# Performance work log

Hardware: AMD Instinct MI355X
Metric: run time of the kernel (lower is better)

The kernel has to match this reference:

```python
import jax, jax.numpy as jnp
import numpy as np
import math

MAX_T = 1000

def _timestep_emb(t, emb_dim):
    half = emb_dim // 2
    freqs = jnp.exp(jnp.arange(half, dtype=jnp.float32) * -(math.log(MAX_T) / (half - 1)))
    e = t.astype(jnp.float32)[:, None] * freqs[None, :]
    return jnp.concatenate([jnp.sin(e), jnp.cos(e)], axis=1)  # [bs, emb_dim]


def setup_inputs() -> dict:
    key = jax.random.key(0)
    ks = jax.random.split(key, 12)
    BS, N, D, H = 16, 1024, 128, 8  # batch, nodes(=in_channels), out_dim(=d), heads
    w = lambda k, shape: jax.random.normal(k, shape, dtype=jnp.float32) * 0.05
    return {
        "A_t": jax.random.normal(ks[0], (BS, N, N), dtype=jnp.float32),
        "F_c": jax.random.normal(ks[1], (BS, N, D), dtype=jnp.float32),
        "t": jax.random.randint(ks[2], (BS,), 0, MAX_T),
        "Wq": w(ks[3], (D, D * H)), "bq": jnp.zeros((D * H,), jnp.float32),
        "Wk": w(ks[4], (D, D * H)), "bk": jnp.zeros((D * H,), jnp.float32),
        "Wv": w(ks[5], (D, D * H)), "bv": jnp.zeros((D * H,), jnp.float32),
        "Wo": w(ks[6], (D * H, D)), "bo": jnp.zeros((D,), jnp.float32),
        "Wg": jnp.eye(D, dtype=jnp.float32),  # GCN weight, eye init
    }


def reference(A_t, F_c, t, Wq, bq, Wk, bk, Wv, bv, Wo, bo, Wg):
    BS, N, D = F_c.shape
    H = Wq.shape[1] // D
    # timestep embedding, emb_dim = in_channels = N
    t_emb = _timestep_emb(t, N)                       # [bs, N]
    c = F_c + t_emb[:, :, None]                       # [bs, N, D]
    # naive multi-head self-attention with per-head dim = out_dim
    q = (c @ Wq + bq).reshape(BS, N, H, D).transpose(0, 2, 1, 3)
    k = (c @ Wk + bk).reshape(BS, N, H, D).transpose(0, 2, 1, 3)
    v = (c @ Wv + bv).reshape(BS, N, H, D).transpose(0, 2, 1, 3)
    scores = jnp.einsum('bhnd,bhmd->bhnm', q, k) / math.sqrt(D)
    a = jax.nn.softmax(scores, axis=-1)
    ctx = jnp.einsum('bhnm,bhmd->bhnd', a, v)
    ctx = ctx.transpose(0, 2, 1, 3).reshape(BS, N, H * D)
    h = ctx @ Wo + bo                                 # [bs, N, D]
    # GCN: relu(A @ (h @ W))
    feat = jax.nn.relu(A_t @ (h @ Wg))                # [bs, N, D]
    # Corr: row-normalize (unbiased std, matching torch.std) then bmm
    mu = feat.mean(axis=-1, keepdims=True)
    std = jnp.std(feat, axis=-1, ddof=1, keepdims=True)
    norm = (feat - mu) / (std + 1e-8)
    return jnp.einsum('bnd,bmd->bnm', norm, norm) / feat.shape[-1]
```

## Files before the change

kernel.cpp:

```cpp
#include <hip/hip_runtime.h>
#include <math.h>

#define NN 1024
#define DD 128
#define HH 8

typedef __attribute__((ext_vector_type(8))) short short8;
typedef __attribute__((ext_vector_type(4))) float f32x4;

__device__ inline unsigned short f2bf(float x) {
    union { float f; unsigned u; } v; v.f = x;
    return (unsigned short)((v.u + 0x7FFF + ((v.u >> 16) & 1)) >> 16);
}
__device__ inline unsigned pack2(float a, float b) {
    return (unsigned)f2bf(a) | ((unsigned)f2bf(b) << 16);
}

__global__ __launch_bounds__(256) void k_prep_w(
    const float* __restrict__ Wq, const float* __restrict__ Wk, const float* __restrict__ Wv,
    const float* __restrict__ Wo, const float* __restrict__ Wg,
    unsigned short* WqT, unsigned short* WkT, unsigned short* WvT,
    unsigned short* WoT, unsigned short* WgT) {
    int id = blockIdx.x;
    const float* src; unsigned short* dst; int R, C, ti;
    if (id < 128)      { src = Wq; dst = WqT; R = 128;  C = 1024; ti = id; }
    else if (id < 256) { src = Wk; dst = WkT; R = 128;  C = 1024; ti = id - 128; }
    else if (id < 384) { src = Wv; dst = WvT; R = 128;  C = 1024; ti = id - 256; }
    else if (id < 512) { src = Wo; dst = WoT; R = 1024; C = 128;  ti = id - 384; }
    else               { src = Wg; dst = WgT; R = 128;  C = 128;  ti = id - 512; }
    int tc = C >> 5;
    int r0 = (ti / tc) << 5, c0 = (ti % tc) << 5;
    __shared__ float T[32][33];
    int tid = threadIdx.x;
    int r = tid >> 3, c4 = (tid & 7) << 2;
    float4 v = *(const float4*)&src[(size_t)(r0 + r) * C + c0 + c4];
    T[r][c4] = v.x; T[r][c4 + 1] = v.y; T[r][c4 + 2] = v.z; T[r][c4 + 3] = v.w;
    __syncthreads();
    int c = tid >> 3, r4 = (tid & 7) << 2;
    uint2 o;
    o.x = pack2(T[r4][c], T[r4 + 1][c]);
    o.y = pack2(T[r4 + 2][c], T[r4 + 3][c]);
    *(uint2*)&dst[(size_t)(c0 + c) * R + r0 + r4] = o;
}

__global__ __launch_bounds__(256) void k_embed(const float* __restrict__ F_c,
                                               const int* __restrict__ t,
                                               unsigned short* __restrict__ cb) {
    int gi = blockIdx.x * 256 + threadIdx.x;
    int row = gi >> 4, ch = gi & 15;
    int b = row >> 10, n = row & 1023;
    float tv = (float)t[b];
    int j = n & 511;
    float e = tv * expf(-(float)j * 0.013518112092919054f);
    float emb = (n < 512) ? sinf(e) : cosf(e);
    const float* src = F_c + (size_t)row * 128 + ch * 8;
    float4 a = *(const float4*)src;
    float4 c4 = *(const float4*)(src + 4);
    uint4 o;
    o.x = pack2(a.x + emb, a.y + emb);  o.y = pack2(a.z + emb, a.w + emb);
    o.z = pack2(c4.x + emb, c4.y + emb); o.w = pack2(c4.z + emb, c4.w + emb);
    *(uint4*)&cb[(size_t)row * 128 + ch * 8] = o;
}

__device__ __forceinline__ void proj_body(const unsigned short* __restrict__ Ain,
                                          const unsigned short* __restrict__ WT,
                                          const float* __restrict__ bias,
                                          unsigned short* __restrict__ Out,
                                          float scale, int mode, int bh_mul,
                                          unsigned short* sm, int head, int m0) {
    unsigned short* CT  = sm;
    unsigned short* WTs = sm + 128 * 136;
    int tid = threadIdx.x;
    int w = tid >> 6, lane = tid & 63, n16 = lane & 15, quad = lane >> 4;
#pragma unroll
    for (int p = 0; p < 8; ++p) {
        int idx = tid + p * 256;
        int r = idx >> 4, ch = idx & 15;
        *(uint4*)&CT[r * 136 + ch * 8]  = *(const uint4*)&Ain[(size_t)(m0 + r) * 128 + ch * 8];
        *(uint4*)&WTs[r * 136 + ch * 8] = *(const uint4*)&WT[(size_t)(head * 128 + r) * 128 + ch * 8];
    }
    __syncthreads();
    int wr = (w >> 1) * 64, wc = (w & 1) * 64;
    f32x4 acc[4][4];
#pragma unroll
    for (int i = 0; i < 4; i++)
#pragma unroll
        for (int j = 0; j < 4; j++) acc[i][j] = (f32x4){0.f, 0.f, 0.f, 0.f};
#pragma unroll
    for (int kk = 0; kk < 4; ++kk) {
        short8 af[4], bf[4];
#pragma unroll
        for (int rb = 0; rb < 4; ++rb)
            af[rb] = *(const short8*)&CT[(wr + rb * 16 + n16) * 136 + kk * 32 + quad * 8];
#pragma unroll
        for (int cb = 0; cb < 4; ++cb)
            bf[cb] = *(const short8*)&WTs[(wc + cb * 16 + n16) * 136 + kk * 32 + quad * 8];
#pragma unroll
        for (int rb = 0; rb < 4; ++rb)
#pragma unroll
            for (int cb = 0; cb < 4; ++cb)
                acc[rb][cb] = __builtin_amdgcn_mfma_f32_16x16x32_bf16(af[rb], bf[cb], acc[rb][cb], 0, 0, 0);
    }
    __syncthreads();
#pragma unroll
    for (int rb = 0; rb < 4; ++rb)
#pragma unroll
        for (int cb = 0; cb < 4; ++cb) {
            int colb = wc + cb * 16 + n16;
            float bs = bias ? bias[head * 128 + colb] : 0.f;
#pragma unroll
            for (int reg = 0; reg < 4; ++reg) {
                int rowb = wr + rb * 16 + quad * 4 + reg;
                unsigned short val = f2bf((acc[rb][cb][reg] + bs) * scale);
                if (mode == 0) CT[rowb * 136 + colb] = val;
                else           CT[colb * 136 + rowb] = val;
            }
        }
    __syncthreads();
    int b = m0 >> 10, n0 = m0 & 1023;
    size_t base = (size_t)(b * bh_mul + head) * 131072;
    if (mode == 0) {
#pragma unroll
        for (int p = 0; p < 8; ++p) {
            int idx = tid + p * 256;
            int r = idx >> 4, ch = idx & 15;
            *(uint4*)&Out[base + (size_t)(n0 + r) * 128 + ch * 8] = *(const uint4*)&CT[r * 136 + ch * 8];
        }
    } else {
#pragma unroll
        for (int p = 0; p < 8; ++p) {
            int idx = tid + p * 256;
            int r = idx >> 4, ch = idx & 15;
            *(uint4*)&Out[base + (size_t)r * 1024 + n0 + ch * 8] = *(const uint4*)&CT[r * 136 + ch * 8];
        }
    }
}

__global__ __launch_bounds__(256) void k_proj_qkv(const unsigned short* __restrict__ Ain,
                                                  const unsigned short* __restrict__ W0,
                                                  const unsigned short* __restrict__ W1,
                                                  const unsigned short* __restrict__ W2,
                                                  const float* __restrict__ b0,
                                                  const float* __restrict__ b1,
                                                  const float* __restrict__ b2,
                                                  unsigned short* __restrict__ O0,
                                                  unsigned short* __restrict__ O1,
                                                  unsigned short* __restrict__ O2,
                                                  float qscale) {
    __shared__ __align__(16) unsigned short sm[2 * 128 * 136];
    int z = blockIdx.z;
    const unsigned short* WT = (z == 0) ? W0 : (z == 1) ? W1 : W2;
    const float* bias = (z == 0) ? b0 : (z == 1) ? b1 : b2;
    unsigned short* Out = (z == 0) ? O0 : (z == 1) ? O1 : O2;
    float scale = (z == 0) ? qscale : 1.f;
    int mode = (z == 2) ? 1 : 0;
    proj_body(Ain, WT, bias, Out, scale, mode, 8, sm, blockIdx.y, blockIdx.x * 128);
}

__global__ __launch_bounds__(256) void k_proj(const unsigned short* __restrict__ Ain,
                                              const unsigned short* __restrict__ WT,
                                              const float* __restrict__ bias,
                                              unsigned short* __restrict__ Out,
                                              float scale, int mode, int bh_mul) {
    __shared__ __align__(16) unsigned short sm[2 * 128 * 136];
    proj_body(Ain, WT, bias, Out, scale, mode, bh_mul, sm, blockIdx.y, blockIdx.x * 128);
}

__device__ __forceinline__ void attn_compute(const unsigned short* __restrict__ Ksc,
                                             const unsigned short* __restrict__ Vtc,
                                             const short8 (&qf)[2][4],
                                             float (&mrun)[2], float (&lrun)[2],
                                             f32x4 (&O)[2][8], int n16, int quad) {
    f32x4 S[2][4];
#pragma unroll
    for (int qb2 = 0; qb2 < 2; ++qb2)
#pragma unroll
        for (int kb = 0; kb < 4; ++kb) S[qb2][kb] = (f32x4){0.f, 0.f, 0.f, 0.f};
    __builtin_amdgcn_s_setprio(1);
#pragma unroll
    for (int kb = 0; kb < 4; ++kb)
#pragma unroll
        for (int dc = 0; dc < 4; ++dc) {
            short8 kf = *(const short8*)&Ksc[(kb * 16 + n16) * 136 + dc * 32 + quad * 8];
            S[0][kb] = __builtin_amdgcn_mfma_f32_16x16x32_bf16(kf, qf[0][dc], S[0][kb], 0, 0, 0);
            S[1][kb] = __builtin_amdgcn_mfma_f32_16x16x32_bf16(kf, qf[1][dc], S[1][kb], 0, 0, 0);
        }
    __builtin_amdgcn_s_setprio(0);

    float mx[2];
#pragma unroll
    for (int qb2 = 0; qb2 < 2; ++qb2) {
        float m = S[qb2][0][0];
#pragma unroll
        for (int kb = 0; kb < 4; ++kb)
#pragma unroll
            for (int reg = 0; reg < 4; ++reg) m = fmaxf(m, S[qb2][kb][reg]);
        m = fmaxf(m, __shfl_xor(m, 16));
        m = fmaxf(m, __shfl_xor(m, 32));
        mx[qb2] = m;
    }
    int keep = (mx[0] - mrun[0] <= 1.f) && (mx[1] - mrun[1] <= 1.f);
    if (!__all(keep)) {
        float mn0 = fmaxf(mrun[0], mx[0]);
        float mn1 = fmaxf(mrun[1], mx[1]);
        float a0 = __expf(mrun[0] - mn0);
        float a1 = __expf(mrun[1] - mn1);
        mrun[0] = mn0; mrun[1] = mn1;
        lrun[0] *= a0; lrun[1] *= a1;
        float av0[4], av1[4];
#pragma unroll
        for (int reg = 0; reg < 4; ++reg) {
            av0[reg] = __shfl(a0, quad * 4 + reg);
            av1[reg] = __shfl(a1, quad * 4 + reg);
        }
#pragma unroll
        for (int dc = 0; dc < 8; ++dc)
#pragma unroll
            for (int reg = 0; reg < 4; ++reg) {
                O[0][dc][reg] *= av0[reg];
                O[1][dc][reg] *= av1[reg];
            }
    }
#pragma unroll
    for (int qb2 = 0; qb2 < 2; ++qb2) {
        float ps = 0.f;
#pragma unroll
        for (int kb = 0; kb < 4; ++kb)
#pragma unroll
            for (int reg = 0; reg < 4; ++reg) {
                float p = __expf(S[qb2][kb][reg] - mrun[qb2]);
                S[qb2][kb][reg] = p;
                ps += p;
            }
        ps += __shfl_xor(ps, 16);
        ps += __shfl_xor(ps, 32);
        lrun[qb2] += ps;
    }
    unsigned pk01[2][4], pk23[2][4];
#pragma unroll
    for (int qb2 = 0; qb2 < 2; ++qb2)
#pragma unroll
        for (int kb = 0; kb < 4; ++kb) {
            asm("v_cvt_pk_bf16_f32 %0, %1, %2"
                : "=v"(pk01[qb2][kb]) : "v"(S[qb2][kb][0]), "v"(S[qb2][kb][1]));
            asm("v_cvt_pk_bf16_f32 %0, %1, %2"
                : "=v"(pk23[qb2][kb]) : "v"(S[qb2][kb][2]), "v"(S[qb2][kb][3]));
        }
    __builtin_amdgcn_s_setprio(1);
#pragma unroll
    for (int c = 0; c < 2; ++c) {
        union { uint4 u; short8 s; } pa0, pa1;
        pa0.u = make_uint4(pk01[0][2 * c], pk23[0][2 * c], pk01[0][2 * c + 1], pk23[0][2 * c + 1]);
        pa1.u = make_uint4(pk01[1][2 * c], pk23[1][2 * c], pk01[1][2 * c + 1], pk23[1][2 * c + 1]);
#pragma unroll
        for (int dc = 0; dc < 8; ++dc) {
            short8 vf = *(const short8*)&Vtc[(dc * 16 + n16) * 72 + c * 32 + quad * 8];
            O[0][dc] = __builtin_amdgcn_mfma_f32_16x16x32_bf16(pa0.s, vf, O[0][dc], 0, 0, 0);
            O[1][dc] = __builtin_amdgcn_mfma_f32_16x16x32_bf16(pa1.s, vf, O[1][dc], 0, 0, 0);
        }
    }
    __builtin_amdgcn_s_setprio(0);
}

__global__ __launch_bounds__(256, 2) void k_attn2(const unsigned short* __restrict__ qbuf,
                                                  const unsigned short* __restrict__ kbuf,
                                                  const unsigned short* __restrict__ vtb,
                                                  unsigned short* __restrict__ ctxb) {
    __shared__ __align__(16) unsigned short sm[35840];
    const int tid = threadIdx.x;
    const int w = tid >> 6, lane = tid & 63;
    const int n16 = lane & 15, quad = lane >> 4;
    const int g = blockIdx.x;
    const int bh = g & 127, tileq = g >> 7;

    const unsigned short* Qp = qbuf + (size_t)bh * 131072 + (size_t)tileq * 16384;
    const unsigned short* Kp = kbuf + (size_t)bh * 131072;
    const unsigned short* Vp = vtb + (size_t)bh * 131072;

    short8 qf[2][4];
#pragma unroll
    for (int qb2 = 0; qb2 < 2; ++qb2)
#pragma unroll
        for (int dc = 0; dc < 4; ++dc)
            qf[qb2][dc] = *(const short8*)&Qp[(size_t)(w * 32 + qb2 * 16 + n16) * 128 + dc * 32 + quad * 8];

    float mrun[2] = {-1e30f, -1e30f};
    float lrun[2] = {0.f, 0.f};
    f32x4 O[2][8];
#pragma unroll
    for (int qb2 = 0; qb2 < 2; ++qb2)
#pragma unroll
        for (int dc = 0; dc < 8; ++dc) O[qb2][dc] = (f32x4){0.f, 0.f, 0.f, 0.f};

    const int vr0 = tid >> 3;
    const int k0 = (tid & 7) * 8;
    const int slotA = ((k0 >> 5) << 5) | (((k0 >> 2) & 3) << 3) | (((k0 >> 4) & 1) << 2);

    uint4 ka[4], va[4];
#pragma unroll
    for (int p = 0; p < 4; ++p) {
        int idx = tid + p * 256;
        int r = idx >> 4, ch = idx & 15;
        ka[p] = *(const uint4*)&Kp[(size_t)r * 128 + ch * 8];
        va[p] = *(const uint4*)&Vp[(size_t)(vr0 + p * 32) * 1024 + k0];
    }
    {
        unsigned short* Kw = sm;
        unsigned short* Vw = sm + 8704;
#pragma unroll
        for (int p = 0; p < 4; ++p) {
            int idx = tid + p * 256;
            int r = idx >> 4, ch = idx & 15;
            *(uint4*)&Kw[r * 136 + ch * 8] = ka[p];
        }
#pragma unroll
        for (int p = 0; p < 4; ++p) {
            int r = vr0 + p * 32;
            *(uint2*)&Vw[r * 72 + slotA]     = make_uint2(va[p].x, va[p].y);
            *(uint2*)&Vw[r * 72 + slotA + 8] = make_uint2(va[p].z, va[p].w);
        }
    }
    __syncthreads();

    for (int kt = 0; kt < 16; ++kt) {
        if (kt < 15) {
#pragma unroll
            for (int p = 0; p < 4; ++p) {
                int idx = tid + p * 256;
                int r = idx >> 4, ch = idx & 15;
                ka[p] = *(const uint4*)&Kp[(size_t)((kt + 1) * 64 + r) * 128 + ch * 8];
                va[p] = *(const uint4*)&Vp[(size_t)(vr0 + p * 32) * 1024 + (kt + 1) * 64 + k0];
            }
        }
        {
            const unsigned short* Ksc = sm + (kt & 1) * 17920;
            const unsigned short* Vtc = Ksc + 8704;
            attn_compute(Ksc, Vtc, qf, mrun, lrun, O, n16, quad);
        }
        if (kt < 15) {
            unsigned short* Kw = sm + ((kt + 1) & 1) * 17920;
            unsigned short* Vw = Kw + 8704;
#pragma unroll
            for (int p = 0; p < 4; ++p) {
                int idx = tid + p * 256;
                int r = idx >> 4, ch = idx & 15;
                *(uint4*)&Kw[r * 136 + ch * 8] = ka[p];
            }
#pragma unroll
            for (int p = 0; p < 4; ++p) {
                int r = vr0 + p * 32;
                *(uint2*)&Vw[r * 72 + slotA]     = make_uint2(va[p].x, va[p].y);
                *(uint2*)&Vw[r * 72 + slotA + 8] = make_uint2(va[p].z, va[p].w);
            }
        }
        __syncthreads();
    }

    float lv[2][4];
#pragma unroll
    for (int qb2 = 0; qb2 < 2; ++qb2)
#pragma unroll
        for (int reg = 0; reg < 4; ++reg)
            lv[qb2][reg] = 1.f / __shfl(lrun[qb2], quad * 4 + reg);
    unsigned short* Ct = sm;
#pragma unroll
    for (int qb2 = 0; qb2 < 2; ++qb2)
#pragma unroll
        for (int reg = 0; reg < 4; ++reg) {
            int row = w * 32 + qb2 * 16 + quad * 4 + reg;
#pragma unroll
            for (int dc = 0; dc < 8; ++dc)
                Ct[row * 136 + dc * 16 + n16] = f2bf(O[qb2][dc][reg] * lv[qb2][reg]);
        }
    __syncthreads();
    unsigned short* Outp = ctxb + (size_t)bh * 131072 + (size_t)tileq * 16384;
#pragma unroll
    for (int p = 0; p < 8; ++p) {
        int idx = tid + p * 256;
        int r = idx >> 4, ch = idx & 15;
        *(uint4*)&Outp[(size_t)r * 128 + ch * 8] = *(const uint4*)&Ct[r * 136 + ch * 8];
    }
}

__global__ __launch_bounds__(256) void k_proj_o(const unsigned short* __restrict__ Ctxb,
                                                const unsigned short* __restrict__ WoT,
                                                const float* __restrict__ bo,
                                                unsigned short* __restrict__ Hb) {
    __shared__ __align__(16) unsigned short sm[2 * 13824];
    int tid = threadIdx.x;
    int m0 = blockIdx.x * 64;
    int b = m0 >> 10, n0 = m0 & 1023;
    int w = tid >> 6, lane = tid & 63, n16 = lane & 15, quad = lane >> 4;
    int wr = (w & 1) * 32, wc = (w >> 1) * 64;
    int r8 = tid >> 3, ch8 = tid & 7;
    f32x4 acc[2][4];
#pragma unroll
    for (int i = 0; i < 2; i++)
#pragma unroll
        for (int j = 0; j < 4; j++) acc[i][j] = (f32x4){0.f, 0.f, 0.f, 0.f};
    uint4 aR[2], bR[4];
#pragma unroll
    for (int p = 0; p < 2; ++p)
        aR[p] = *(const uint4*)&Ctxb[((size_t)(b * 8) * 1024 + n0 + r8 + p * 32) * 128 + ch8 * 8];
#pragma unroll
    for (int p = 0; p < 4; ++p)
        bR[p] = *(const uint4*)&WoT[(size_t)(r8 + p * 32) * 1024 + ch8 * 8];
    {
        unsigned short* As = sm;
        unsigned short* Bs = sm + 64 * 72;
#pragma unroll
        for (int p = 0; p < 2; ++p) *(uint4*)&As[(r8 + p * 32) * 72 + ch8 * 8] = aR[p];
#pragma unroll
        for (int p = 0; p < 4; ++p) *(uint4*)&Bs[(r8 + p * 32) * 72 + ch8 * 8] = bR[p];
    }
    __syncthreads();
    for (int kt = 0; kt < 16; ++kt) {
        if (kt < 15) {
            int kn = kt + 1, hh = kn >> 1, d0 = (kn & 1) * 64;
#pragma unroll
            for (int p = 0; p < 2; ++p)
                aR[p] = *(const uint4*)&Ctxb[((size_t)(b * 8 + hh) * 1024 + n0 + r8 + p * 32) * 128 + d0 + ch8 * 8];
#pragma unroll
            for (int p = 0; p < 4; ++p)
                bR[p] = *(const uint4*)&WoT[(size_t)(r8 + p * 32) * 1024 + kn * 64 + ch8 * 8];
        }
        const unsigned short* As = sm + (kt & 1) * 13824;
        const unsigned short* Bs = As + 64 * 72;
#pragma unroll
        for (int kk = 0; kk < 2; ++kk) {
            short8 af0 = *(const short8*)&As[(wr + n16) * 72 + kk * 32 + quad * 8];
            short8 af1 = *(const short8*)&As[(wr + 16 + n16) * 72 + kk * 32 + quad * 8];
#pragma unroll
            for (int cb = 0; cb < 4; ++cb) {
                short8 bf = *(const short8*)&Bs[(wc + cb * 16 + n16) * 72 + kk * 32 + quad * 8];
                acc[0][cb] = __builtin_amdgcn_mfma_f32_16x16x32_bf16(af0, bf, acc[0][cb], 0, 0, 0);
                acc[1][cb] = __builtin_amdgcn_mfma_f32_16x16x32_bf16(af1, bf, acc[1][cb], 0, 0, 0);
            }
        }
        if (kt < 15) {
            unsigned short* Aw = sm + ((kt + 1) & 1) * 13824;
            unsigned short* Bw = Aw + 64 * 72;
#pragma unroll
            for (int p = 0; p < 2; ++p) *(uint4*)&Aw[(r8 + p * 32) * 72 + ch8 * 8] = aR[p];
#pragma unroll
            for (int p = 0; p < 4; ++p) *(uint4*)&Bw[(r8 + p * 32) * 72 + ch8 * 8] = bR[p];
        }
        __syncthreads();
    }
    unsigned short* Ct = sm;
#pragma unroll
    for (int rb = 0; rb < 2; ++rb)
#pragma unroll
        for (int cb = 0; cb < 4; ++cb) {
            int col = wc + cb * 16 + n16;
            float bs = bo[col];
#pragma unroll
            for (int reg = 0; reg < 4; ++reg)
                Ct[(wr + rb * 16 + quad * 4 + reg) * 136 + col] = f2bf(acc[rb][cb][reg] + bs);
        }
    __syncthreads();
#pragma unroll
    for (int p = 0; p < 4; ++p) {
        int idx = tid + p * 256;
        int r = idx >> 4, ch = idx & 15;
        *(uint4*)&Hb[(size_t)(m0 + r) * 128 + ch * 8] = *(const uint4*)&Ct[r * 136 + ch * 8];
    }
}

__global__ __launch_bounds__(256) void k_at_gemm(const float* __restrict__ At,
                                                 const unsigned short* __restrict__ HgT,
                                                 float* __restrict__ Feat) {
    __shared__ __align__(16) unsigned short sm[2 * 13824];
    int tid = threadIdx.x;
    int bz = blockIdx.z;
    int m0 = blockIdx.x * 64;
    int w = tid >> 6, lane = tid & 63, n16 = lane & 15, quad = lane >> 4;
    int wr = (w & 1) * 32, wc = (w >> 1) * 64;
    int r8 = tid >> 3, ch8 = tid & 7;
    f32x4 acc[2][4];
#pragma unroll
    for (int i = 0; i < 2; i++)
#pragma unroll
        for (int j = 0; j < 4; j++) acc[i][j] = (f32x4){0.f, 0.f, 0.f, 0.f};
    float4 axR[2], ayR[2]; uint4 bR[4];
#pragma unroll
    for (int p = 0; p < 2; ++p) {
        const float* s = At + (size_t)bz * 1048576 + (size_t)(m0 + r8 + p * 32) * 1024 + ch8 * 8;
        axR[p] = *(const float4*)s;
        ayR[p] = *(const float4*)(s + 4);
    }
#pragma unroll
    for (int p = 0; p < 4; ++p)
        bR[p] = *(const uint4*)&HgT[(size_t)bz * 131072 + (size_t)(r8 + p * 32) * 1024 + ch8 * 8];
    {
        unsigned short* As = sm;
        unsigned short* Bs = sm + 64 * 72;
#pragma unroll
        for (int p = 0; p < 2; ++p) {
            uint4 o;
            o.x = pack2(axR[p].x, axR[p].y); o.y = pack2(axR[p].z, axR[p].w);
            o.z = pack2(ayR[p].x, ayR[p].y); o.w = pack2(ayR[p].z, ayR[p].w);
            *(uint4*)&As[(r8 + p * 32) * 72 + ch8 * 8] = o;
        }
#pragma unroll
        for (int p = 0; p < 4; ++p) *(uint4*)&Bs[(r8 + p * 32) * 72 + ch8 * 8] = bR[p];
    }
    __syncthreads();
    for (int kt = 0; kt < 16; ++kt) {
        if (kt < 15) {
            int kn = kt + 1;
#pragma unroll
            for (int p = 0; p < 2; ++p) {
                const float* s = At + (size_t)bz * 1048576 + (size_t)(m0 + r8 + p * 32) * 1024 + kn * 64 + ch8 * 8;
                axR[p] = *(const float4*)s;
                ayR[p] = *(const float4*)(s + 4);
            }
#pragma unroll
            for (int p = 0; p < 4; ++p)
                bR[p] = *(const uint4*)&HgT[(size_t)bz * 131072 + (size_t)(r8 + p * 32) * 1024 + kn * 64 + ch8 * 8];
        }
        const unsigned short* As = sm + (kt & 1) * 13824;
        const unsigned short* Bs = As + 64 * 72;
#pragma unroll
        for (int kk = 0; kk < 2; ++kk) {
            short8 af0 = *(const short8*)&As[(wr + n16) * 72 + kk * 32 + quad * 8];
            short8 af1 = *(const short8*)&As[(wr + 16 + n16) * 72 + kk * 32 + quad * 8];
#pragma unroll
            for (int cb = 0; cb < 4; ++cb) {
                short8 bf = *(const short8*)&Bs[(wc + cb * 16 + n16) * 72 + kk * 32 + quad * 8];
                acc[0][cb] = __builtin_amdgcn_mfma_f32_16x16x32_bf16(af0, bf, acc[0][cb], 0, 0, 0);
                acc[1][cb] = __builtin_amdgcn_mfma_f32_16x16x32_bf16(af1, bf, acc[1][cb], 0, 0, 0);
            }
        }
        if (kt < 15) {
            unsigned short* Aw = sm + ((kt + 1) & 1) * 13824;
            unsigned short* Bw = Aw + 64 * 72;
#pragma unroll
            for (int p = 0; p < 2; ++p) {
                uint4 o;
                o.x = pack2(axR[p].x, axR[p].y); o.y = pack2(axR[p].z, axR[p].w);
                o.z = pack2(ayR[p].x, ayR[p].y); o.w = pack2(ayR[p].z, ayR[p].w);
                *(uint4*)&Aw[(r8 + p * 32) * 72 + ch8 * 8] = o;
            }
#pragma unroll
            for (int p = 0; p < 4; ++p) *(uint4*)&Bw[(r8 + p * 32) * 72 + ch8 * 8] = bR[p];
        }
        __syncthreads();
    }
#pragma unroll
    for (int rb = 0; rb < 2; ++rb)
#pragma unroll
        for (int cb = 0; cb < 4; ++cb) {
            int col = wc + cb * 16 + n16;
#pragma unroll
            for (int reg = 0; reg < 4; ++reg) {
                int row = m0 + wr + rb * 16 + quad * 4 + reg;
                Feat[(size_t)bz * 131072 + (size_t)row * 128 + col] = fmaxf(acc[rb][cb][reg], 0.f);
            }
        }
}

__global__ __launch_bounds__(64) void k_norm(const float* __restrict__ F,
                                             unsigned short* __restrict__ Nb) {
    int row = blockIdx.x, tdx = threadIdx.x;
    const float* p = F + (size_t)row * 128;
    float2 xy = *(const float2*)&p[tdx * 2];
    float sum = xy.x + xy.y;
#pragma unroll
    for (int off = 32; off; off >>= 1) sum += __shfl_xor(sum, off);
    float mu = sum * (1.f / 128.f);
    float d0 = xy.x - mu, d1 = xy.y - mu;
    float sq = d0 * d0 + d1 * d1;
#pragma unroll
    for (int off = 32; off; off >>= 1) sq += __shfl_xor(sq, off);
    float sd = sqrtf(sq * (1.f / 127.f));
    float inv = 1.f / (sd + 1e-8f);
    ((unsigned*)Nb)[(size_t)row * 64 + tdx] = pack2(d0 * inv, d1 * inv);
}

__global__ __launch_bounds__(256) void k_corr(const unsigned short* __restrict__ Nb,
                                              float* __restrict__ Out) {
    __shared__ __align__(16) unsigned short sm[2 * 128 * 136];
    unsigned short* Ar = sm;
    unsigned short* Br = sm + 128 * 136;
    int tid = threadIdx.x;
    int bz = blockIdx.z;
    int n0 = blockIdx.x * 128, m0 = blockIdx.y * 128;
    const unsigned short* base = Nb + (size_t)bz * 131072;
    int w = tid >> 6, lane = tid & 63, n16 = lane & 15, quad = lane >> 4;
#pragma unroll
    for (int p = 0; p < 8; ++p) {
        int idx = tid + p * 256;
        int r = idx >> 4, ch = idx & 15;
        *(uint4*)&Ar[r * 136 + ch * 8] = *(const uint4*)&base[(size_t)(n0 + r) * 128 + ch * 8];
        *(uint4*)&Br[r * 136 + ch * 8] = *(const uint4*)&base[(size_t)(m0 + r) * 128 + ch * 8];
    }
    __syncthreads();
    int wr = (w >> 1) * 64, wc = (w & 1) * 64;
    f32x4 acc[4][4];
#pragma unroll
    for (int i = 0; i < 4; i++)
#pragma unroll
        for (int j = 0; j < 4; j++) acc[i][j] = (f32x4){0.f, 0.f, 0.f, 0.f};
#pragma unroll
    for (int kk = 0; kk < 4; ++kk) {
        short8 af[4], bf[4];
#pragma unroll
        for (int rb = 0; rb < 4; ++rb)
            af[rb] = *(const short8*)&Ar[(wr + rb * 16 + n16) * 136 + kk * 32 + quad * 8];
#pragma unroll
        for (int cb = 0; cb < 4; ++cb)
            bf[cb] = *(const short8*)&Br[(wc + cb * 16 + n16) * 136 + kk * 32 + quad * 8];
#pragma unroll
        for (int rb = 0; rb < 4; ++rb)
#pragma unroll
            for (int cb = 0; cb < 4; ++cb)
                acc[rb][cb] = __builtin_amdgcn_mfma_f32_16x16x32_bf16(af[rb], bf[cb], acc[rb][cb], 0, 0, 0);
    }
#pragma unroll
    for (int rb = 0; rb < 4; ++rb)
#pragma unroll
        for (int cb = 0; cb < 4; ++cb)
#pragma unroll
            for (int reg = 0; reg < 4; ++reg) {
                int row = n0 + wr + rb * 16 + quad * 4 + reg;
                int col = m0 + wc + cb * 16 + n16;
                Out[(size_t)bz * 1048576 + (size_t)row * 1024 + col] = acc[rb][cb][reg] * 0.0078125f;
            }
}

extern "C" void kernel_launch(void* const* d_in, const int* in_sizes, int n_in,
                              void* d_out, int out_size, void* d_ws, size_t ws_size,
                              hipStream_t stream) {
    const float* A_t = (const float*)d_in[0];
    const float* F_c = (const float*)d_in[1];
    const int*   t   = (const int*)d_in[2];
    const float* Wq  = (const float*)d_in[3];
    const float* bq  = (const float*)d_in[4];
    const float* Wk  = (const float*)d_in[5];
    const float* bk  = (const float*)d_in[6];
    const float* Wv  = (const float*)d_in[7];
    const float* bv  = (const float*)d_in[8];
    const float* Wo  = (const float*)d_in[9];
    const float* bo  = (const float*)d_in[10];
    const float* Wg  = (const float*)d_in[11];
    float* out = (float*)d_out;
    char* ws = (char*)d_ws;

    unsigned short* cb   = (unsigned short*)(ws);
    unsigned short* qb   = (unsigned short*)(ws + 4194304);
    unsigned short* kbuf = (unsigned short*)(ws + 37748736);
    unsigned short* vtb  = (unsigned short*)(ws + 71303168);
    unsigned short* ctxb = (unsigned short*)(ws + 104857600);
    unsigned short* hb   = (unsigned short*)(ws + 138412032);
    unsigned short* hgT  = (unsigned short*)(ws + 142606336);
    float*          feat = (float*)        (ws + 146800640);
    unsigned short* nb   = (unsigned short*)(ws + 155189248);
    unsigned short* WqT  = (unsigned short*)(ws + 159383552);
    unsigned short* WkT  = (unsigned short*)(ws + 159645696);
    unsigned short* WvT  = (unsigned short*)(ws + 159907840);
    unsigned short* WoT  = (unsigned short*)(ws + 160169984);
    unsigned short* WgT  = (unsigned short*)(ws + 160432128);

    const float qscale = 0.08838834764831845f;

    k_prep_w<<<528, 256, 0, stream>>>(Wq, Wk, Wv, Wo, Wg, WqT, WkT, WvT, WoT, WgT);
    k_embed<<<1024, 256, 0, stream>>>(F_c, t, cb);
    k_proj_qkv<<<dim3(128, 8, 3), 256, 0, stream>>>(cb, WqT, WkT, WvT, bq, bk, bv,
                                                    qb, kbuf, vtb, qscale);
    k_attn2<<<1024, 256, 0, stream>>>(qb, kbuf, vtb, ctxb);
    k_proj_o<<<256, 256, 0, stream>>>(ctxb, WoT, bo, hb);
    k_proj<<<dim3(128, 1), 256, 0, stream>>>(hb, WgT, nullptr, hgT, 1.f, 1, 1);
    k_at_gemm<<<dim3(16, 1, 16), 256, 0, stream>>>(A_t, hgT, feat);
    k_norm<<<16384, 64, 0, stream>>>(feat, nb);
    k_corr<<<dim3(8, 8, 16), 256, 0, stream>>>(nb, out);
}
```

Measured before the change: 325.1 us.

## Software-pipeline attention: overlap next tile's QK MFMA with current softmax/PV

The flash-attention loop is split into a QK^T stage and a softmax+PV stage and rearranged so the QK scores for tile k+1 are computed while softmax and PV run for tile k. K and V staging is offset, with V kept one tile behind K in separate register buffers and LDS slots. The aim is to keep the MFMA units busy across the softmax dependency chain. In exchange it holds two score tiles and an extra V register set live, which raises register pressure and may lower occupancy, and it adds a barrier before the epilogue reuses LDS.

```diff
diff --git a/kernel.cpp b/kernel.cpp
--- a/kernel.cpp
+++ b/kernel.cpp
@@ -166,12 +166,9 @@
     proj_body(Ain, WT, bias, Out, scale, mode, bh_mul, sm, blockIdx.y, blockIdx.x * 128);
 }
 
-__device__ __forceinline__ void attn_compute(const unsigned short* __restrict__ Ksc,
-                                             const unsigned short* __restrict__ Vtc,
-                                             const short8 (&qf)[2][4],
-                                             float (&mrun)[2], float (&lrun)[2],
-                                             f32x4 (&O)[2][8], int n16, int quad) {
-    f32x4 S[2][4];
+__device__ __forceinline__ void attn_qk(const unsigned short* __restrict__ Ksc,
+                                        const short8 (&qf)[2][4],
+                                        f32x4 (&S)[2][4], int n16, int quad) {
 #pragma unroll
     for (int qb2 = 0; qb2 < 2; ++qb2)
 #pragma unroll
@@ -186,7 +183,12 @@
             S[1][kb] = __builtin_amdgcn_mfma_f32_16x16x32_bf16(kf, qf[1][dc], S[1][kb], 0, 0, 0);
         }
     __builtin_amdgcn_s_setprio(0);
-
+}
+
+__device__ __forceinline__ void attn_sm_pv(f32x4 (&S)[2][4],
+                                           const unsigned short* __restrict__ Vtc,
+                                           float (&mrun)[2], float (&lrun)[2],
+                                           f32x4 (&O)[2][8], int n16, int quad) {
     float mx[2];
 #pragma unroll
     for (int qb2 = 0; qb2 < 2; ++qb2) {
@@ -295,66 +297,67 @@
     const int vr0 = tid >> 3;
     const int k0 = (tid & 7) * 8;
     const int slotA = ((k0 >> 5) << 5) | (((k0 >> 2) & 3) << 3) | (((k0 >> 4) & 1) << 2);
-
-    uint4 ka[4], va[4];
-#pragma unroll
-    for (int p = 0; p < 4; ++p) {
-        int idx = tid + p * 256;
-        int r = idx >> 4, ch = idx & 15;
-        ka[p] = *(const uint4*)&Kp[(size_t)r * 128 + ch * 8];
-        va[p] = *(const uint4*)&Vp[(size_t)(vr0 + p * 32) * 1024 + k0];
-    }
-    {
-        unsigned short* Kw = sm;
-        unsigned short* Vw = sm + 8704;
-#pragma unroll
-        for (int p = 0; p < 4; ++p) {
-            int idx = tid + p * 256;
-            int r = idx >> 4, ch = idx & 15;
-            *(uint4*)&Kw[r * 136 + ch * 8] = ka[p];
-        }
-#pragma unroll
-        for (int p = 0; p < 4; ++p) {
-            int r = vr0 + p * 32;
-            *(uint2*)&Vw[r * 72 + slotA]     = make_uint2(va[p].x, va[p].y);
-            *(uint2*)&Vw[r * 72 + slotA + 8] = make_uint2(va[p].z, va[p].w);
-        }
-    }
-    __syncthreads();
-
-    for (int kt = 0; kt < 16; ++kt) {
-        if (kt < 15) {
-#pragma unroll
-            for (int p = 0; p < 4; ++p) {
-                int idx = tid + p * 256;
-                int r = idx >> 4, ch = idx & 15;
-                ka[p] = *(const uint4*)&Kp[(size_t)((kt + 1) * 64 + r) * 128 + ch * 8];
-                va[p] = *(const uint4*)&Vp[(size_t)(vr0 + p * 32) * 1024 + (kt + 1) * 64 + k0];
-            }
-        }
-        {
-            const unsigned short* Ksc = sm + (kt & 1) * 17920;
-            const unsigned short* Vtc = Ksc + 8704;
-            attn_compute(Ksc, Vtc, qf, mrun, lrun, O, n16, quad);
-        }
-        if (kt < 15) {
-            unsigned short* Kw = sm + ((kt + 1) & 1) * 17920;
-            unsigned short* Vw = Kw + 8704;
-#pragma unroll
-            for (int p = 0; p < 4; ++p) {
-                int idx = tid + p * 256;
-                int r = idx >> 4, ch = idx & 15;
-                *(uint4*)&Kw[r * 136 + ch * 8] = ka[p];
-            }
-#pragma unroll
-            for (int p = 0; p < 4; ++p) {
-                int r = vr0 + p * 32;
-                *(uint2*)&Vw[r * 72 + slotA]     = make_uint2(va[p].x, va[p].y);
-                *(uint2*)&Vw[r * 72 + slotA + 8] = make_uint2(va[p].z, va[p].w);
-            }
-        }
+    const int kr = tid >> 4, kch = tid & 15;
+
+    unsigned short* Kb0 = sm;
+    unsigned short* Vb0 = sm + 8704;
+    unsigned short* Kb1 = sm + 17920;
+    unsigned short* Vb1 = sm + 17920 + 8704;
+
+    uint4 ka[4], va0[4], va1[4];
+    f32x4 Sa[2][4], Sb[2][4];
+
+#define LOADK(dst, kt_) _Pragma("unroll") \
+    for (int p = 0; p < 4; ++p) \
+        dst[p] = *(const uint4*)&Kp[(size_t)((kt_) * 64 + kr + p * 16) * 128 + kch * 8];
+#define LOADV(dst, kt_) _Pragma("unroll") \
+    for (int p = 0; p < 4; ++p) \
+        dst[p] = *(const uint4*)&Vp[(size_t)(vr0 + p * 32) * 1024 + (kt_) * 64 + k0];
+#define WRITEK(buf, src) _Pragma("unroll") \
+    for (int p = 0; p < 4; ++p) \
+        *(uint4*)&buf[(kr + p * 16) * 136 + kch * 8] = src[p];
+#define WRITEV(buf, src) _Pragma("unroll") \
+    for (int p = 0; p < 4; ++p) { \
+        int r = vr0 + p * 32; \
+        *(uint2*)&buf[r * 72 + slotA]     = make_uint2(src[p].x, src[p].y); \
+        *(uint2*)&buf[r * 72 + slotA + 8] = make_uint2(src[p].z, src[p].w); \
+    }
+
+    LOADK(ka, 0); LOADV(va0, 0);
+    WRITEK(Kb0, ka); WRITEV(Vb0, va0);
+    __syncthreads();
+
+    LOADK(ka, 1); LOADV(va1, 1);
+    attn_qk(Kb0, qf, Sa, n16, quad);
+    WRITEK(Kb1, ka);
+    __syncthreads();
+
+#pragma unroll 1
+    for (int t = 0; t < 7; ++t) {
+        int ko = 2 * t + 1;
+        LOADK(ka, ko + 1); LOADV(va0, ko + 1);
+        attn_qk(Kb1, qf, Sb, n16, quad);
+        attn_sm_pv(Sa, Vb0, mrun, lrun, O, n16, quad);
+        WRITEK(Kb0, ka);
+        WRITEV(Vb1, va1);
         __syncthreads();
-    }
+        LOADK(ka, ko + 2); LOADV(va1, ko + 2);
+        attn_qk(Kb0, qf, Sa, n16, quad);
+        attn_sm_pv(Sb, Vb1, mrun, lrun, O, n16, quad);
+        WRITEK(Kb1, ka);
+        WRITEV(Vb0, va0);
+        __syncthreads();
+    }
+    attn_qk(Kb1, qf, Sb, n16, quad);
+    attn_sm_pv(Sa, Vb0, mrun, lrun, O, n16, quad);
+    WRITEV(Vb1, va1);
+    __syncthreads();
+    attn_sm_pv(Sb, Vb1, mrun, lrun, O, n16, quad);
+
+#undef LOADK
+#undef LOADV
+#undef WRITEK
+#undef WRITEV
 
     float lv[2][4];
 #pragma unroll
@@ -362,6 +365,7 @@
 #pragma unroll
         for (int reg = 0; reg < 4; ++reg)
             lv[qb2][reg] = 1.f / __shfl(lrun[qb2], quad * 4 + reg);
+    __syncthreads();
     unsigned short* Ct = sm;
 #pragma unroll
     for (int qb2 = 0; qb2 < 2; ++qb2)
```

Measured after the change: 328.0 us. Within noise of the previous version (+0.9%).
